# Kernel tuning notes

Measured on AMD Instinct MI355X. Metric: run time of the kernel, lower is better.

Reference implementation:

```python
import jax, jax.numpy as jnp
import numpy as np

NHEAD = 4
NLAYERS = 4
C = 128
EPS = 1e-5


def ln(x, g, b):
    m = x.mean(-1, keepdims=True)
    v = jnp.var(x, axis=-1, keepdims=True)
    return (x - m) / jnp.sqrt(v + EPS) * g + b


def mha_rel(q_in, k_in, in_w, in_b, out_w, out_b, pos_enc, pos_idx, self_attn):
    # q_in/k_in: [W, N, C]; pos_enc: [2W-1, C]; pos_idx: [W*W] int
    w, bsz, c = q_in.shape
    hd = c // NHEAD
    scale = hd ** -0.5
    if self_attn:
        qkv = q_in @ in_w.T + in_b
        q, k, v = jnp.split(qkv, 3, axis=-1)
    else:
        q = q_in @ in_w[:c].T + in_b[:c]
        kv = k_in @ in_w[c:].T + in_b[c:]
        k, v = jnp.split(kv, 2, axis=-1)
    pe = pos_enc[pos_idx].reshape(w, w, c)             # [W, W', C] gathered rel-pos
    qr_kr = pe @ in_w[:2 * c].T + in_b[:2 * c]
    q_r, k_r = jnp.split(qr_kr, 2, axis=-1)
    q = (q * scale).reshape(w, bsz, NHEAD, hd)
    q_r = (q_r * scale).reshape(w, w, NHEAD, hd)
    k = k.reshape(w, bsz, NHEAD, hd)
    v = v.reshape(w, bsz, NHEAD, hd)
    k_r = k_r.reshape(w, w, NHEAD, hd)
    # content-content + content-pos + pos-content (STTR MultiheadAttentionRelative)
    attn = (jnp.einsum('wnec,vnec->newv', q, k)
            + jnp.einsum('wnec,wvec->newv', q, k_r)
            + jnp.einsum('vnec,wvec->newv', k, q_r))   # [N, E, W, W']
    raw = attn.sum(1)
    a = jax.nn.softmax(attn, axis=-1)
    v_o = jnp.einsum('newv,vnec->wnec', a, v).reshape(w, bsz, c)
    v_o = v_o @ out_w.T + out_b
    return v_o, a.sum(1) / NHEAD, raw


def _forward(feat_left, feat_right, pos_enc,
             s_iw, s_ib, s_ow, s_ob, s_g, s_b,
             c_iw, c_ib, c_ow, c_ob, c_g1, c_b1, c_g2, c_b2):
    bs, c, hn0, w = feat_left.shape
    hn = hn0 * bs

    def to_seq(x):  # [bs,c,hn,w] -> [w, hn*bs, c]
        return jnp.transpose(jnp.transpose(x, (1, 3, 2, 0)).reshape(c, w, hn), (1, 2, 0))

    fl = to_seq(feat_left)
    fr = to_seq(feat_right)
    pos_idx = (jnp.arange(w - 1, -1, -1)[:, None] + jnp.arange(w)[None, :]).reshape(-1)
    pos_flip = pos_enc[::-1]
    feat = jnp.concatenate([fl, fr], axis=1)           # [w, 2hn, c]
    for i in range(NLAYERS):
        # self attention over concatenated left/right
        f2 = ln(feat, s_g[i], s_b[i])
        f2, _, _ = mha_rel(f2, f2, s_iw[i], s_ib[i], s_ow[i], s_ob[i], pos_enc, pos_idx, True)
        feat = feat + f2
        # cross attention
        fl, fr = feat[:, :hn], feat[:, hn:]
        fl2 = ln(fl, c_g1[i], c_b1[i])
        fr2 = ln(fr, c_g1[i], c_b1[i])
        fr2u, _, _ = mha_rel(fr2, fl2, c_iw[i], c_ib[i], c_ow[i], c_ob[i], pos_flip, pos_idx, False)
        fr = fr + fr2u
        fr2n = ln(fr, c_g2[i], c_b2[i])
        fl2u, _, _ = mha_rel(fl2, fr2n, c_iw[i], c_ib[i], c_ow[i], c_ob[i], pos_enc, pos_idx, False)
        fl = fl + fl2u
        feat = jnp.concatenate([fl, fr], axis=1)
    return feat


def setup_inputs() -> dict:
    key = jax.random.key(0)
    ks = jax.random.split(key, 20)
    bs, hn, w = 2, 64, 192
    p = 0.02
    return {
        "feat_left": jax.random.normal(ks[0], (bs, C, hn, w), jnp.float32),
        "feat_right": jax.random.normal(ks[1], (bs, C, hn, w), jnp.float32),
        "pos_enc": jax.random.normal(ks[2], (2 * w - 1, C), jnp.float32),
        "s_iw": jax.random.normal(ks[3], (NLAYERS, 3 * C, C), jnp.float32) * p,
        "s_ib": jax.random.normal(ks[4], (NLAYERS, 3 * C), jnp.float32) * p,
        "s_ow": jax.random.normal(ks[5], (NLAYERS, C, C), jnp.float32) * p,
        "s_ob": jax.random.normal(ks[6], (NLAYERS, C), jnp.float32) * p,
        "s_g": jnp.ones((NLAYERS, C), jnp.float32),
        "s_b": jnp.zeros((NLAYERS, C), jnp.float32),
        "c_iw": jax.random.normal(ks[7], (NLAYERS, 3 * C, C), jnp.float32) * p,
        "c_ib": jax.random.normal(ks[8], (NLAYERS, 3 * C), jnp.float32) * p,
        "c_ow": jax.random.normal(ks[9], (NLAYERS, C, C), jnp.float32) * p,
        "c_ob": jax.random.normal(ks[10], (NLAYERS, C), jnp.float32) * p,
        "c_g1": jnp.ones((NLAYERS, C), jnp.float32),
        "c_b1": jnp.zeros((NLAYERS, C), jnp.float32),
        "c_g2": jnp.ones((NLAYERS, C), jnp.float32),
        "c_b2": jnp.zeros((NLAYERS, C), jnp.float32),
    }


def reference(feat_left, feat_right, pos_enc,
              s_iw, s_ib, s_ow, s_ob, s_g, s_b,
              c_iw, c_ib, c_ow, c_ob, c_g1, c_b1, c_g2, c_b2):
    return _forward(feat_left, feat_right, pos_enc,
                    s_iw, s_ib, s_ow, s_ob, s_g, s_b,
                    c_iw, c_ib, c_ow, c_ob, c_g1, c_b1, c_g2, c_b2)
```

## Files before the change

### kernel.cpp

```cpp
#include <hip/hip_runtime.h>
#include <hip/hip_bf16.h>
#include <math.h>

#define WW 192
#define NTOT 256
#define HNN 128
#define CC 128
#define NH 4
#define NLAY 4
#define EPSF 1e-5f
#define SCALE 0.17677669529663687f

typedef __attribute__((ext_vector_type(8))) short short8_t;
typedef __attribute__((ext_vector_type(4))) float f32x4;

#define MFMA(a, b, c) __builtin_amdgcn_mfma_f32_16x16x32_bf16(a, b, c, 0, 0, 0)

__device__ __forceinline__ ushort f2b(float f) {
  union { float f; uint u; } x; x.f = f;
  uint r = x.u + 0x7fffu + ((x.u >> 16) & 1u);
  return (ushort)(r >> 16);
}

__global__ __launch_bounds__(256) void k_build_feat(const float* __restrict__ L,
                                                    const float* __restrict__ R,
                                                    float* __restrict__ feat) {
  __shared__ float tile[32][33];
  int wt = blockIdx.x, h0 = blockIdx.y, z = blockIdx.z;
  int ct = z & 3, b = (z >> 2) & 1, side = z >> 3;
  const float* src = side ? R : L;
  int tx = threadIdx.x & 31, ty = threadIdx.x >> 5;
  const float* sp = src + ((size_t)(b * 128 + ct * 32) * 64 + h0) * 192 + wt * 32;
  #pragma unroll
  for (int yy = 0; yy < 4; ++yy) {
    int c = ty * 4 + yy;
    tile[c][tx] = sp[(size_t)c * 64 * 192 + tx];
  }
  __syncthreads();
  int n = 2 * h0 + b + side * 128;
  #pragma unroll
  for (int yy = 0; yy < 4; ++yy) {
    int w = ty * 4 + yy;
    feat[((size_t)(wt * 32 + w) * 256 + n) * 128 + ct * 32 + tx] = tile[tx][w];
  }
}

__global__ __launch_bounds__(256) void k_gemm_mfma(
    const void* __restrict__ Xv, int lnmode, int xN, int x0,
    const float* __restrict__ lng, const float* __restrict__ lnb,
    const float* __restrict__ Wt, const float* __restrict__ bias,
    void* __restrict__ Yv, int yN, int y0, int ystride, int yf32res,
    int T, int nsub, float* __restrict__ Ymir) {
  extern __shared__ char smem[];
  ushort* As = (ushort*)smem;
  ushort* Bs = As + 128 * 128;
  float* biasS = (float*)(Bs + 128 * 128);

  int bm = blockIdx.x, bn = blockIdx.y;
  int tid = threadIdx.x;

  {
    int row = tid >> 1;
    int ce0 = (tid & 1) * 64;
    int t = bm * 128 + row;
    bool ok = (t < T);
    int w = 0, h = 0;
    if (ok) { w = t / nsub; h = t - w * nsub; }
    if (lnmode) {
      const float* src = (const float*)Xv + (size_t)(w * xN + x0 + h) * CC + ce0;
      float vals[64];
      float s = 0.f, s2 = 0.f;
      #pragma unroll
      for (int i = 0; i < 16; ++i) {
        float4 v = ok ? *(const float4*)(src + i * 4) : make_float4(0.f, 0.f, 0.f, 0.f);
        vals[i * 4 + 0] = v.x; vals[i * 4 + 1] = v.y;
        vals[i * 4 + 2] = v.z; vals[i * 4 + 3] = v.w;
        s += v.x + v.y + v.z + v.w;
        s2 += v.x * v.x + v.y * v.y + v.z * v.z + v.w * v.w;
      }
      s += __shfl_xor(s, 1);
      s2 += __shfl_xor(s2, 1);
      float m = s * (1.0f / 128.0f);
      float inv = rsqrtf(s2 * (1.0f / 128.0f) - m * m + EPSF);
      #pragma unroll
      for (int i = 0; i < 8; ++i) {
        float4 g0 = *(const float4*)(lng + ce0 + i * 8);
        float4 g1 = *(const float4*)(lng + ce0 + i * 8 + 4);
        float4 b0 = *(const float4*)(lnb + ce0 + i * 8);
        float4 b1 = *(const float4*)(lnb + ce0 + i * 8 + 4);
        short8_t pv;
        pv[0] = (short)f2b((vals[i * 8 + 0] - m) * inv * g0.x + b0.x);
        pv[1] = (short)f2b((vals[i * 8 + 1] - m) * inv * g0.y + b0.y);
        pv[2] = (short)f2b((vals[i * 8 + 2] - m) * inv * g0.z + b0.z);
        pv[3] = (short)f2b((vals[i * 8 + 3] - m) * inv * g0.w + b0.w);
        pv[4] = (short)f2b((vals[i * 8 + 4] - m) * inv * g1.x + b1.x);
        pv[5] = (short)f2b((vals[i * 8 + 5] - m) * inv * g1.y + b1.y);
        pv[6] = (short)f2b((vals[i * 8 + 6] - m) * inv * g1.z + b1.z);
        pv[7] = (short)f2b((vals[i * 8 + 7] - m) * inv * g1.w + b1.w);
        int cb = (ce0 + i * 8) * 2;
        *(short8_t*)((char*)As + row * 256 + (cb ^ ((row & 7) << 4))) = pv;
      }
    } else {
      const ushort* src = (const ushort*)Xv + (size_t)(w * xN + x0 + h) * CC + ce0;
      #pragma unroll
      for (int i = 0; i < 8; ++i) {
        short8_t v = {};
        if (ok) v = *(const short8_t*)(src + i * 8);
        int cb = (ce0 + i * 8) * 2;
        *(short8_t*)((char*)As + row * 256 + (cb ^ ((row & 7) << 4))) = v;
      }
    }
    const float* wsrc = Wt + (size_t)(bn * 128 + row) * CC + ce0;
    #pragma unroll
    for (int i = 0; i < 8; ++i) {
      float4 v0 = *(const float4*)(wsrc + i * 8);
      float4 v1 = *(const float4*)(wsrc + i * 8 + 4);
      short8_t pv;
      pv[0] = (short)f2b(v0.x); pv[1] = (short)f2b(v0.y);
      pv[2] = (short)f2b(v0.z); pv[3] = (short)f2b(v0.w);
      pv[4] = (short)f2b(v1.x); pv[5] = (short)f2b(v1.y);
      pv[6] = (short)f2b(v1.z); pv[7] = (short)f2b(v1.w);
      int cb = (ce0 + i * 8) * 2;
      *(short8_t*)((char*)Bs + row * 256 + (cb ^ ((row & 7) << 4))) = pv;
    }
    if (tid < 128) biasS[tid] = bias[bn * 128 + tid];
  }
  __syncthreads();

  int lane = tid & 63, wid = tid >> 6;
  int wm = (wid >> 1) * 64, wn = (wid & 1) * 64;
  int r = lane & 15, g = lane >> 4;

  f32x4 acc[4][4] = {};
  #pragma unroll
  for (int kc = 0; kc < 4; ++kc) {
    short8_t af[4], bf[4];
    #pragma unroll
    for (int mt = 0; mt < 4; ++mt) {
      int row = wm + mt * 16 + r;
      af[mt] = *(const short8_t*)((const char*)As + row * 256 + ((kc * 64 + g * 16) ^ ((row & 7) << 4)));
    }
    #pragma unroll
    for (int nt = 0; nt < 4; ++nt) {
      int row = wn + nt * 16 + r;
      bf[nt] = *(const short8_t*)((const char*)Bs + row * 256 + ((kc * 64 + g * 16) ^ ((row & 7) << 4)));
    }
    __builtin_amdgcn_s_setprio(1);
    #pragma unroll
    for (int mt = 0; mt < 4; ++mt)
      #pragma unroll
      for (int nt = 0; nt < 4; ++nt)
        acc[mt][nt] = MFMA(af[mt], bf[nt], acc[mt][nt]);
    __builtin_amdgcn_s_setprio(0);
  }

  #pragma unroll
  for (int mt = 0; mt < 4; ++mt) {
    #pragma unroll
    for (int reg = 0; reg < 4; ++reg) {
      int t = bm * 128 + wm + mt * 16 + g * 4 + reg;
      if (t < T) {
        int w = t / nsub, h = t - w * nsub;
        size_t ybase = (size_t)(w * yN + y0 + h) * ystride + bn * 128;
        #pragma unroll
        for (int nt = 0; nt < 4; ++nt) {
          int nn = wn + nt * 16 + r;
          float v = acc[mt][nt][reg] + biasS[nn];
          if (yf32res) {
            float nv = ((float*)Yv)[ybase + nn] + v;
            ((float*)Yv)[ybase + nn] = nv;
            if (Ymir) Ymir[ybase + nn] = nv;
          } else {
            ((ushort*)Yv)[ybase + nn] = f2b(v);
          }
        }
      }
    }
  }
}

__global__ __launch_bounds__(256) void k_rr(
    const float* __restrict__ pos_enc,
    const float* __restrict__ s_iw, const float* __restrict__ s_ib,
    const float* __restrict__ c_iw, const float* __restrict__ c_ib,
    ushort* __restrict__ out_all) {
  extern __shared__ char smem[];
  ushort* As = (ushort*)smem;
  ushort* Bs = As + 128 * 128;
  float* biasS = (float*)(Bs + 128 * 128);

  int bm = blockIdx.x, bn = blockIdx.y, z = blockIdx.z;
  int layer = z >> 1;
  const float* Wt = ((z & 1) ? c_iw : s_iw) + (size_t)layer * 384 * CC;
  const float* bias = ((z & 1) ? c_ib : s_ib) + layer * 384;
  ushort* out = out_all + (size_t)z * 383 * 256;
  int tid = threadIdx.x;

  {
    int row = tid >> 1;
    int ce0 = (tid & 1) * 64;
    int t = bm * 128 + row;
    bool ok = (t < 383);
    const float* src = pos_enc + (size_t)t * CC + ce0;
    #pragma unroll
    for (int i = 0; i < 8; ++i) {
      float4 v0 = ok ? *(const float4*)(src + i * 8) : make_float4(0.f, 0.f, 0.f, 0.f);
      float4 v1 = ok ? *(const float4*)(src + i * 8 + 4) : make_float4(0.f, 0.f, 0.f, 0.f);
      short8_t pv;
      pv[0] = (short)f2b(v0.x); pv[1] = (short)f2b(v0.y);
      pv[2] = (short)f2b(v0.z); pv[3] = (short)f2b(v0.w);
      pv[4] = (short)f2b(v1.x); pv[5] = (short)f2b(v1.y);
      pv[6] = (short)f2b(v1.z); pv[7] = (short)f2b(v1.w);
      int cb = (ce0 + i * 8) * 2;
      *(short8_t*)((char*)As + row * 256 + (cb ^ ((row & 7) << 4))) = pv;
    }
    const float* wsrc = Wt + (size_t)(bn * 128 + row) * CC + ce0;
    #pragma unroll
    for (int i = 0; i < 8; ++i) {
      float4 v0 = *(const float4*)(wsrc + i * 8);
      float4 v1 = *(const float4*)(wsrc + i * 8 + 4);
      short8_t pv;
      pv[0] = (short)f2b(v0.x); pv[1] = (short)f2b(v0.y);
      pv[2] = (short)f2b(v0.z); pv[3] = (short)f2b(v0.w);
      pv[4] = (short)f2b(v1.x); pv[5] = (short)f2b(v1.y);
      pv[6] = (short)f2b(v1.z); pv[7] = (short)f2b(v1.w);
      int cb = (ce0 + i * 8) * 2;
      *(short8_t*)((char*)Bs + row * 256 + (cb ^ ((row & 7) << 4))) = pv;
    }
    if (tid < 128) biasS[tid] = bias[bn * 128 + tid];
  }
  __syncthreads();

  int lane = tid & 63, wid = tid >> 6;
  int wm = (wid >> 1) * 64, wn = (wid & 1) * 64;
  int r = lane & 15, g = lane >> 4;

  f32x4 acc[4][4] = {};
  #pragma unroll
  for (int kc = 0; kc < 4; ++kc) {
    short8_t af[4], bf[4];
    #pragma unroll
    for (int mt = 0; mt < 4; ++mt) {
      int row = wm + mt * 16 + r;
      af[mt] = *(const short8_t*)((const char*)As + row * 256 + ((kc * 64 + g * 16) ^ ((row & 7) << 4)));
    }
    #pragma unroll
    for (int nt = 0; nt < 4; ++nt) {
      int row = wn + nt * 16 + r;
      bf[nt] = *(const short8_t*)((const char*)Bs + row * 256 + ((kc * 64 + g * 16) ^ ((row & 7) << 4)));
    }
    #pragma unroll
    for (int mt = 0; mt < 4; ++mt)
      #pragma unroll
      for (int nt = 0; nt < 4; ++nt)
        acc[mt][nt] = MFMA(af[mt], bf[nt], acc[mt][nt]);
  }

  #pragma unroll
  for (int mt = 0; mt < 4; ++mt) {
    #pragma unroll
    for (int reg = 0; reg < 4; ++reg) {
      int t = bm * 128 + wm + mt * 16 + g * 4 + reg;
      if (t < 383) {
        #pragma unroll
        for (int nt = 0; nt < 4; ++nt) {
          int nn = wn + nt * 16 + r;
          out[(size_t)t * 256 + bn * 128 + nn] = f2b(acc[mt][nt][reg] + biasS[nn]);
        }
      }
    }
  }
}

#define KS_ST 36
#define VT_ST 196
#define B2_ST 37
#define PL_ST 20

template <int SGN>
__global__ __launch_bounds__(256, 4) void k_attn_mfma(
    const ushort* __restrict__ qbuf, int qstride, int qoff, int qN, int qn0,
    const ushort* __restrict__ kvbuf, int kvstride, int koff, int voff, int kN, int kn0,
    const ushort* __restrict__ rrb,
    ushort* __restrict__ obuf, int oN,
    int nblk) {
  __shared__ ushort Ks[192 * KS_ST];
  __shared__ ushort Vt[32 * VT_ST];
  __shared__ float Sb[4 * 16 * B2_ST];
  __shared__ uint PLb[4 * 16 * PL_ST];

  int bid = blockIdx.x;
  int n = bid % nblk;
  int rest = bid / nblk;
  int h = rest & 3;
  int ts = rest >> 2;
  int tid = threadIdx.x;
  int lane = tid & 63, wid = tid >> 6;
  int r = lane & 15, g = lane >> 4;
  int g4 = g * 4;

  for (int i = tid; i < 768; i += 256) {
    int row = i >> 2, c8 = (i & 3) * 8;
    *(short8_t*)&Ks[row * KS_ST + c8] =
        *(const short8_t*)(kvbuf + (size_t)(row * kN + kn0 + n) * kvstride + koff + h * 32 + c8);
  }
  {
    uint* Vtu = (uint*)Vt;
    for (int i = tid; i < 384; i += 256) {
      int dg = i / 96;
      int p = i - dg * 96;
      const ushort* vb = kvbuf + (size_t)((2 * p) * kN + kn0 + n) * kvstride + voff + h * 32 + dg * 8;
      short8_t a = *(const short8_t*)vb;
      short8_t b = *(const short8_t*)(vb + (size_t)kN * kvstride);
      #pragma unroll
      for (int j = 0; j < 8; ++j)
        Vtu[(dg * 8 + j) * 98 + p] = ((uint)(ushort)a[j]) | (((uint)(ushort)b[j]) << 16);
    }
  }
  int w0 = (ts * 4 + wid) * 16;
  short8_t qf = *(const short8_t*)(qbuf + (size_t)((w0 + r) * qN + qn0 + n) * qstride + qoff + h * 32 + g * 8);
  __syncthreads();

  float* flat = Sb + wid * 16 * B2_ST;
  uint* PL = PLb + wid * 16 * PL_ST;
  const ushort* KRg = rrb + 128 + h * 32 + g * 8;
  const ushort* QRg = rrb + h * 32 + g * 8;
  const f32x4 zf = {0.f, 0.f, 0.f, 0.f};

  int ca = (SGN < 0) ? (r + 1) : (31 - r);
  int cbn = (SGN < 0) ? (17 + r) : (15 - r);
  int rdcol = 16 - r + g4;

  f32x4 esum = zf, o0 = zf, o1 = zf;

  #pragma unroll
  for (int vp = 0; vp < 6; ++vp) {
    #pragma unroll
    for (int half = 0; half < 2; ++half) {
      int s = 2 * vp + half;
      int v0 = s * 16;
      short8_t kf = *(const short8_t*)&Ks[(v0 + r) * KS_ST + g * 8];
      int base2 = 176 + SGN * (w0 - v0);
      const ushort* krp = KRg + (size_t)(base2 + r) * 256;
      const ushort* qrp = QRg + (size_t)(base2 + r) * 256;
      short8_t krf0 = *(const short8_t*)krp;
      short8_t krf1 = *(const short8_t*)(krp + 16 * 256);
      short8_t qrf0 = *(const short8_t*)qrp;
      short8_t qrf1 = *(const short8_t*)(qrp + 16 * 256);
      __builtin_amdgcn_s_setprio(1);
      f32x4 t1  = MFMA(kf, qf, zf);
      f32x4 t3a = MFMA(kf, qrf0, zf);
      f32x4 t3b = MFMA(kf, qrf1, zf);
      f32x4 t2a = MFMA(qf, krf0, zf);
      f32x4 t2b = MFMA(qf, krf1, zf);
      __builtin_amdgcn_s_setprio(0);
      #pragma unroll
      for (int reg = 0; reg < 4; ++reg) {
        flat[(g4 + reg) * B2_ST + ca] = t2a[reg];
        flat[(g4 + reg) * B2_ST + cbn] = t2b[reg];
      }
      f32x4 p2v = *(const f32x4*)&flat[r * B2_ST + rdcol];
      f32x4 ev;
      #pragma unroll
      for (int reg = 0; reg < 4; ++reg) {
        int js = 15 + SGN * (r - g4 - reg);
        int idx = (lane & 48) | (js & 15);
        float v3a = __shfl(t3a[reg], idx);
        float v3b = __shfl(t3b[reg], idx);
        float p3 = (js < 16) ? v3a : v3b;
        float e = __expf((t1[reg] + p2v[reg] + p3) * SCALE);
        ev[reg] = e;
        esum[reg] += e;
      }
      uint pa = (uint)f2b(ev[0]) | ((uint)f2b(ev[1]) << 16);
      uint pbu = (uint)f2b(ev[2]) | ((uint)f2b(ev[3]) << 16);
      *(uint2*)&PL[r * PL_ST + 8 * half + 2 * g] = make_uint2(pa, pbu);
    }
    union { uint u[4]; short8_t s8; } pb;
    uint4 pr = *(const uint4*)&PL[r * PL_ST + 4 * g];
    pb.u[0] = pr.x; pb.u[1] = pr.y; pb.u[2] = pr.z; pb.u[3] = pr.w;
    short8_t vt0 = *(const short8_t*)&Vt[r * VT_ST + vp * 32 + g * 8];
    short8_t vt1 = *(const short8_t*)&Vt[(16 + r) * VT_ST + vp * 32 + g * 8];
    __builtin_amdgcn_s_setprio(1);
    o0 = MFMA(vt0, pb.s8, o0);
    o1 = MFMA(vt1, pb.s8, o1);
    __builtin_amdgcn_s_setprio(0);
  }

  float ssum = (esum[0] + esum[1]) + (esum[2] + esum[3]);
  ssum += __shfl_xor(ssum, 16);
  ssum += __shfl_xor(ssum, 32);

  float inv = 1.0f / ssum;
  ushort4 u0, u1;
  u0.x = f2b(o0[0] * inv); u0.y = f2b(o0[1] * inv);
  u0.z = f2b(o0[2] * inv); u0.w = f2b(o0[3] * inv);
  u1.x = f2b(o1[0] * inv); u1.y = f2b(o1[1] * inv);
  u1.z = f2b(o1[2] * inv); u1.w = f2b(o1[3] * inv);
  size_t rowb = (size_t)((w0 + r) * oN + n) * CC + h * 32;
  *(ushort4*)(obuf + rowb + g4) = u0;
  *(ushort4*)(obuf + rowb + 16 + g4) = u1;
}

extern "C" void kernel_launch(void* const* d_in, const int* in_sizes, int n_in,
                              void* d_out, int out_size, void* d_ws, size_t ws_size,
                              hipStream_t stream) {
  const float* feat_left  = (const float*)d_in[0];
  const float* feat_right = (const float*)d_in[1];
  const float* pos_enc    = (const float*)d_in[2];
  const float* s_iw = (const float*)d_in[3];
  const float* s_ib = (const float*)d_in[4];
  const float* s_ow = (const float*)d_in[5];
  const float* s_ob = (const float*)d_in[6];
  const float* s_g  = (const float*)d_in[7];
  const float* s_b  = (const float*)d_in[8];
  const float* c_iw = (const float*)d_in[9];
  const float* c_ib = (const float*)d_in[10];
  const float* c_ow = (const float*)d_in[11];
  const float* c_ob = (const float*)d_in[12];
  const float* c_g1 = (const float*)d_in[13];
  const float* c_b1 = (const float*)d_in[14];
  const float* c_g2 = (const float*)d_in[15];
  const float* c_b2 = (const float*)d_in[16];

  char* W = (char*)d_ws;
  const int FEAT_N = WW * NTOT * CC;
  float*  feat    = (float*)W;
  ushort* qkv     = (ushort*)(W + 25165824);
  ushort* obuf    = (ushort*)(W + 62914560);
  ushort* kv2     = (ushort*)(W + 75497472);
  ushort* rrb_all = (ushort*)(W + 88080384);

  const int GEMM_LDS = 128 * 128 * 2 * 2 + 128 * 4;
  hipFuncSetAttribute(reinterpret_cast<const void*>(&k_gemm_mfma),
                      hipFuncAttributeMaxDynamicSharedMemorySize, GEMM_LDS);
  hipFuncSetAttribute(reinterpret_cast<const void*>(&k_rr),
                      hipFuncAttributeMaxDynamicSharedMemorySize, GEMM_LDS);

  k_build_feat<<<dim3(6, 64, 16), 256, 0, stream>>>(feat_left, feat_right, feat);
  k_rr<<<dim3(3, 2, 8), 256, GEMM_LDS, stream>>>(pos_enc, s_iw, s_ib, c_iw, c_ib, rrb_all);

  const int T_FULL = WW * NTOT;
  const int T_HALF = WW * HNN;

  for (int i = 0; i < NLAY; ++i) {
    const float* siw = s_iw + (size_t)i * 384 * CC;
    const float* sib = s_ib + i * 384;
    const float* sow = s_ow + (size_t)i * CC * CC;
    const float* sob = s_ob + i * CC;
    const float* ciw = c_iw + (size_t)i * 384 * CC;
    const float* cib = c_ib + i * 384;
    const float* cow = c_ow + (size_t)i * CC * CC;
    const float* cob = c_ob + i * CC;
    const ushort* rr_self  = rrb_all + (size_t)(2 * i) * 383 * 256;
    const ushort* rr_cross = rrb_all + (size_t)(2 * i + 1) * 383 * 256;
    float* mir = (i == NLAY - 1) ? (float*)d_out : nullptr;

    k_gemm_mfma<<<dim3(T_FULL / 128, 3), 256, GEMM_LDS, stream>>>(
        feat, 1, NTOT, 0, s_g + i * CC, s_b + i * CC, siw, sib,
        qkv, NTOT, 0, 384, 0, T_FULL, NTOT, nullptr);
    k_attn_mfma<-1><<<NTOT * NH * 3, 256, 0, stream>>>(
        qkv, 384, 0, NTOT, 0, qkv, 384, 128, 256, NTOT, 0,
        rr_self, obuf, NTOT, NTOT);
    k_gemm_mfma<<<dim3(T_FULL / 128, 1), 256, GEMM_LDS, stream>>>(
        obuf, 0, NTOT, 0, nullptr, nullptr, sow, sob,
        feat, NTOT, 0, CC, 1, T_FULL, NTOT, nullptr);

    k_gemm_mfma<<<dim3(T_FULL / 128, 3), 256, GEMM_LDS, stream>>>(
        feat, 1, NTOT, 0, c_g1 + i * CC, c_b1 + i * CC, ciw, cib,
        qkv, NTOT, 0, 384, 0, T_FULL, NTOT, nullptr);

    k_attn_mfma<+1><<<HNN * NH * 3, 256, 0, stream>>>(
        qkv, 384, 0, NTOT, 128, qkv, 384, 128, 256, NTOT, 0,
        rr_cross, obuf, HNN, HNN);
    k_gemm_mfma<<<dim3(T_HALF / 128, 1), 256, GEMM_LDS, stream>>>(
        obuf, 0, HNN, 0, nullptr, nullptr, cow, cob,
        feat, NTOT, 128, CC, 1, T_HALF, HNN, mir);

    k_gemm_mfma<<<dim3(T_HALF / 128, 2), 256, GEMM_LDS, stream>>>(
        feat, 1, NTOT, 128, c_g2 + i * CC, c_b2 + i * CC, ciw + 128 * CC, cib + 128,
        kv2, HNN, 0, 256, 0, T_HALF, HNN, nullptr);
    k_attn_mfma<-1><<<HNN * NH * 3, 256, 0, stream>>>(
        qkv, 384, 0, NTOT, 0, kv2, 256, 0, 128, HNN, 0,
        rr_cross, obuf, HNN, HNN);
    k_gemm_mfma<<<dim3(T_HALF / 128, 1), 256, GEMM_LDS, stream>>>(
        obuf, 0, HNN, 0, nullptr, nullptr, cow, cob,
        feat, NTOT, 0, CC, 1, T_HALF, HNN, mir);
  }
}
```

Baseline: 1.497 ms.

## Pre-convert weights to bf16 and split LayerNorm out of GEMM

Adds a one-time kernel that converts all projection weights to bf16, so GEMM blocks load bf16 weights directly instead of converting fp32 per block. LayerNorm moves out of the GEMM prologue into a separate k_ln kernel that writes a bf16 normalized buffer, which the GEMM then reads. This drops redundant per-block weight conversion and LN recompute across the column blocks, but adds extra launches and a bf16 activation round-trip through memory.

Measured after the change: 1.382 ms. 1.08x faster.

```diff
diff --git a/kernel.cpp b/kernel.cpp
--- a/kernel.cpp
+++ b/kernel.cpp
@@ -45,10 +45,53 @@
   }
 }
 
-__global__ __launch_bounds__(256) void k_gemm_mfma(
-    const void* __restrict__ Xv, int lnmode, int xN, int x0,
-    const float* __restrict__ lng, const float* __restrict__ lnb,
-    const float* __restrict__ Wt, const float* __restrict__ bias,
+__global__ __launch_bounds__(256) void k_wconv(
+    const float* __restrict__ s_iw, const float* __restrict__ s_ow,
+    const float* __restrict__ c_iw, const float* __restrict__ c_ow,
+    ushort* __restrict__ out) {
+  int i4 = (blockIdx.x * 256 + threadIdx.x) * 4;
+  const float* src;
+  int off;
+  if (i4 < 196608) { src = s_iw; off = i4; }
+  else if (i4 < 262144) { src = s_ow; off = i4 - 196608; }
+  else if (i4 < 458752) { src = c_iw; off = i4 - 262144; }
+  else { src = c_ow; off = i4 - 458752; }
+  float4 v = *(const float4*)(src + off);
+  ushort4 o;
+  o.x = f2b(v.x); o.y = f2b(v.y); o.z = f2b(v.z); o.w = f2b(v.w);
+  *(ushort4*)(out + i4) = o;
+}
+
+__global__ __launch_bounds__(256) void k_ln(const float* __restrict__ src,
+                                            ushort* __restrict__ dst,
+                                            const float* __restrict__ g,
+                                            const float* __restrict__ b,
+                                            int n0, int nsub) {
+  int t = blockIdx.x * 4 + (threadIdx.x >> 6);
+  int lane = threadIdx.x & 63;
+  int w = t / nsub, h = t - w * nsub;
+  size_t row = (size_t)(w * NTOT + n0 + h) * CC;
+  int c0 = lane * 2;
+  float2 x = *(const float2*)(src + row + c0);
+  float s = x.x + x.y;
+  float s2 = x.x * x.x + x.y * x.y;
+  #pragma unroll
+  for (int o = 1; o < 64; o <<= 1) {
+    s += __shfl_xor(s, o);
+    s2 += __shfl_xor(s2, o);
+  }
+  float m = s * (1.0f / 128.0f);
+  float var = s2 * (1.0f / 128.0f) - m * m;
+  float inv = rsqrtf(var + EPSF);
+  float oa = (x.x - m) * inv * g[c0] + b[c0];
+  float ob = (x.y - m) * inv * g[c0 + 1] + b[c0 + 1];
+  uint pack = (uint)f2b(oa) | ((uint)f2b(ob) << 16);
+  *(uint*)(dst + row + c0) = pack;
+}
+
+__global__ __launch_bounds__(256) void k_gemm_bf16(
+    const ushort* __restrict__ X, int xN, int x0,
+    const ushort* __restrict__ Wb, const float* __restrict__ bias,
     void* __restrict__ Yv, int yN, int y0, int ystride, int yf32res,
     int T, int nsub, float* __restrict__ Ymir) {
   extern __shared__ char smem[];
@@ -66,62 +109,20 @@
     bool ok = (t < T);
     int w = 0, h = 0;
     if (ok) { w = t / nsub; h = t - w * nsub; }
-    if (lnmode) {
-      const float* src = (const float*)Xv + (size_t)(w * xN + x0 + h) * CC + ce0;
-      float vals[64];
-      float s = 0.f, s2 = 0.f;
-      #pragma unroll
-      for (int i = 0; i < 16; ++i) {
-        float4 v = ok ? *(const float4*)(src + i * 4) : make_float4(0.f, 0.f, 0.f, 0.f);
-        vals[i * 4 + 0] = v.x; vals[i * 4 + 1] = v.y;
-        vals[i * 4 + 2] = v.z; vals[i * 4 + 3] = v.w;
-        s += v.x + v.y + v.z + v.w;
-        s2 += v.x * v.x + v.y * v.y + v.z * v.z + v.w * v.w;
-      }
-      s += __shfl_xor(s, 1);
-      s2 += __shfl_xor(s2, 1);
-      float m = s * (1.0f / 128.0f);
-      float inv = rsqrtf(s2 * (1.0f / 128.0f) - m * m + EPSF);
-      #pragma unroll
-      for (int i = 0; i < 8; ++i) {
-        float4 g0 = *(const float4*)(lng + ce0 + i * 8);
-        float4 g1 = *(const float4*)(lng + ce0 + i * 8 + 4);
-        float4 b0 = *(const float4*)(lnb + ce0 + i * 8);
-        float4 b1 = *(const float4*)(lnb + ce0 + i * 8 + 4);
-        short8_t pv;
-        pv[0] = (short)f2b((vals[i * 8 + 0] - m) * inv * g0.x + b0.x);
-        pv[1] = (short)f2b((vals[i * 8 + 1] - m) * inv * g0.y + b0.y);
-        pv[2] = (short)f2b((vals[i * 8 + 2] - m) * inv * g0.z + b0.z);
-        pv[3] = (short)f2b((vals[i * 8 + 3] - m) * inv * g0.w + b0.w);
-        pv[4] = (short)f2b((vals[i * 8 + 4] - m) * inv * g1.x + b1.x);
-        pv[5] = (short)f2b((vals[i * 8 + 5] - m) * inv * g1.y + b1.y);
-        pv[6] = (short)f2b((vals[i * 8 + 6] - m) * inv * g1.z + b1.z);
-        pv[7] = (short)f2b((vals[i * 8 + 7] - m) * inv * g1.w + b1.w);
-        int cb = (ce0 + i * 8) * 2;
-        *(short8_t*)((char*)As + row * 256 + (cb ^ ((row & 7) << 4))) = pv;
-      }
-    } else {
-      const ushort* src = (const ushort*)Xv + (size_t)(w * xN + x0 + h) * CC + ce0;
-      #pragma unroll
-      for (int i = 0; i < 8; ++i) {
-        short8_t v = {};
-        if (ok) v = *(const short8_t*)(src + i * 8);
-        int cb = (ce0 + i * 8) * 2;
-        *(short8_t*)((char*)As + row * 256 + (cb ^ ((row & 7) << 4))) = v;
-      }
-    }
-    const float* wsrc = Wt + (size_t)(bn * 128 + row) * CC + ce0;
+    const ushort* src = X + (size_t)(w * xN + x0 + h) * CC + ce0;
     #pragma unroll
     for (int i = 0; i < 8; ++i) {
-      float4 v0 = *(const float4*)(wsrc + i * 8);
-      float4 v1 = *(const float4*)(wsrc + i * 8 + 4);
-      short8_t pv;
-      pv[0] = (short)f2b(v0.x); pv[1] = (short)f2b(v0.y);
-      pv[2] = (short)f2b(v0.z); pv[3] = (short)f2b(v0.w);
-      pv[4] = (short)f2b(v1.x); pv[5] = (short)f2b(v1.y);
-      pv[6] = (short)f2b(v1.z); pv[7] = (short)f2b(v1.w);
+      short8_t v = {};
+      if (ok) v = *(const short8_t*)(src + i * 8);
       int cb = (ce0 + i * 8) * 2;
-      *(short8_t*)((char*)Bs + row * 256 + (cb ^ ((row & 7) << 4))) = pv;
+      *(short8_t*)((char*)As + row * 256 + (cb ^ ((row & 7) << 4))) = v;
+    }
+    const ushort* wsrc = Wb + (size_t)(bn * 128 + row) * CC + ce0;
+    #pragma unroll
+    for (int i = 0; i < 8; ++i) {
+      short8_t v = *(const short8_t*)(wsrc + i * 8);
+      int cb = (ce0 + i * 8) * 2;
+      *(short8_t*)((char*)Bs + row * 256 + (cb ^ ((row & 7) << 4))) = v;
     }
     if (tid < 128) biasS[tid] = bias[bn * 128 + tid];
   }
@@ -426,65 +427,72 @@
   char* W = (char*)d_ws;
   const int FEAT_N = WW * NTOT * CC;
   float*  feat    = (float*)W;
-  ushort* qkv     = (ushort*)(W + 25165824);
-  ushort* obuf    = (ushort*)(W + 62914560);
+  ushort* f2obuf  = (ushort*)(W + 25165824);
+  ushort* qkv     = (ushort*)(W + 37748736);
   ushort* kv2     = (ushort*)(W + 75497472);
   ushort* rrb_all = (ushort*)(W + 88080384);
+  ushort* wbf     = (ushort*)(W + 89649152);
+
+  ushort* f2   = f2obuf;
+  ushort* obuf = f2obuf;
 
   const int GEMM_LDS = 128 * 128 * 2 * 2 + 128 * 4;
-  hipFuncSetAttribute(reinterpret_cast<const void*>(&k_gemm_mfma),
+  hipFuncSetAttribute(reinterpret_cast<const void*>(&k_gemm_bf16),
                       hipFuncAttributeMaxDynamicSharedMemorySize, GEMM_LDS);
   hipFuncSetAttribute(reinterpret_cast<const void*>(&k_rr),
                       hipFuncAttributeMaxDynamicSharedMemorySize, GEMM_LDS);
 
   k_build_feat<<<dim3(6, 64, 16), 256, 0, stream>>>(feat_left, feat_right, feat);
   k_rr<<<dim3(3, 2, 8), 256, GEMM_LDS, stream>>>(pos_enc, s_iw, s_ib, c_iw, c_ib, rrb_all);
+  k_wconv<<<512, 256, 0, stream>>>(s_iw, s_ow, c_iw, c_ow, wbf);
+
+  const ushort* siw_bf_base = wbf;
+  const ushort* sow_bf_base = wbf + 196608;
+  const ushort* ciw_bf_base = wbf + 262144;
+  const ushort* cow_bf_base = wbf + 458752;
 
   const int T_FULL = WW * NTOT;
   const int T_HALF = WW * HNN;
 
   for (int i = 0; i < NLAY; ++i) {
-    const float* siw = s_iw + (size_t)i * 384 * CC;
     const float* sib = s_ib + i * 384;
-    const float* sow = s_ow + (size_t)i * CC * CC;
     const float* sob = s_ob + i * CC;
-    const float* ciw = c_iw + (size_t)i * 384 * CC;
     const float* cib = c_ib + i * 384;
-    const float* cow = c_ow + (size_t)i * CC * CC;
     const float* cob = c_ob + i * CC;
+    const ushort* siw_bf = siw_bf_base + (size_t)i * 384 * CC;
+    const ushort* sow_bf = sow_bf_base + (size_t)i * CC * CC;
+    const ushort* ciw_bf = ciw_bf_base + (size_t)i * 384 * CC;
+    const ushort* cow_bf = cow_bf_base + (size_t)i * CC * CC;
     const ushort* rr_self  = rrb_all + (size_t)(2 * i) * 383 * 256;
     const ushort* rr_cross = rrb_all + (size_t)(2 * i + 1) * 383 * 256;
     float* mir = (i == NLAY - 1) ? (float*)d_out : nullptr;
 
-    k_gemm_mfma<<<dim3(T_FULL / 128, 3), 256, GEMM_LDS, stream>>>(
-        feat, 1, NTOT, 0, s_g + i * CC, s_b + i * CC, siw, sib,
-        qkv, NTOT, 0, 384, 0, T_FULL, NTOT, nullptr);
+    k_ln<<<T_FULL / 4, 256, 0, stream>>>(feat, f2, s_g + i * CC, s_b + i * CC, 0, NTOT);
+    k_gemm_bf16<<<dim3(T_FULL / 128, 3), 256, GEMM_LDS, stream>>>(
+        f2, NTOT, 0, siw_bf, sib, qkv, NTOT, 0, 384, 0, T_FULL, NTOT, nullptr);
     k_attn_mfma<-1><<<NTOT * NH * 3, 256, 0, stream>>>(
         qkv, 384, 0, NTOT, 0, qkv, 384, 128, 256, NTOT, 0,
         rr_self, obuf, NTOT, NTOT);
-    k_gemm_mfma<<<dim3(T_FULL / 128, 1), 256, GEMM_LDS, stream>>>(
-        obuf, 0, NTOT, 0, nullptr, nullptr, sow, sob,
-        feat, NTOT, 0, CC, 1, T_FULL, NTOT, nullptr);
-
-    k_gemm_mfma<<<dim3(T_FULL / 128, 3), 256, GEMM_LDS, stream>>>(
-        feat, 1, NTOT, 0, c_g1 + i * CC, c_b1 + i * CC, ciw, cib,
-        qkv, NTOT, 0, 384, 0, T_FULL, NTOT, nullptr);
+    k_gemm_bf16<<<dim3(T_FULL / 128, 1), 256, GEMM_LDS, stream>>>(
+        obuf, NTOT, 0, sow_bf, sob, feat, NTOT, 0, CC, 1, T_FULL, NTOT, nullptr);
+
+    k_ln<<<T_FULL / 4, 256, 0, stream>>>(feat, f2, c_g1 + i * CC, c_b1 + i * CC, 0, NTOT);
+    k_gemm_bf16<<<dim3(T_FULL / 128, 3), 256, GEMM_LDS, stream>>>(
+        f2, NTOT, 0, ciw_bf, cib, qkv, NTOT, 0, 384, 0, T_FULL, NTOT, nullptr);
 
     k_attn_mfma<+1><<<HNN * NH * 3, 256, 0, stream>>>(
         qkv, 384, 0, NTOT, 128, qkv, 384, 128, 256, NTOT, 0,
         rr_cross, obuf, HNN, HNN);
-    k_gemm_mfma<<<dim3(T_HALF / 128, 1), 256, GEMM_LDS, stream>>>(
-        obuf, 0, HNN, 0, nullptr, nullptr, cow, cob,
-        feat, NTOT, 128, CC, 1, T_HALF, HNN, mir);
-
-    k_gemm_mfma<<<dim3(T_HALF / 128, 2), 256, GEMM_LDS, stream>>>(
-        feat, 1, NTOT, 128, c_g2 + i * CC, c_b2 + i * CC, ciw + 128 * CC, cib + 128,
-        kv2, HNN, 0, 256, 0, T_HALF, HNN, nullptr);
+    k_gemm_bf16<<<dim3(T_HALF / 128, 1), 256, GEMM_LDS, stream>>>(
+        obuf, HNN, 0, cow_bf, cob, feat, NTOT, 128, CC, 1, T_HALF, HNN, mir);
+
+    k_ln<<<T_HALF / 4, 256, 0, stream>>>(feat, f2, c_g2 + i * CC, c_b2 + i * CC, 128, HNN);
+    k_gemm_bf16<<<dim3(T_HALF / 128, 2), 256, GEMM_LDS, stream>>>(
+        f2, NTOT, 128, ciw_bf + 128 * CC, cib + 128, kv2, HNN, 0, 256, 0, T_HALF, HNN, nullptr);
     k_attn_mfma<-1><<<HNN * NH * 3, 256, 0, stream>>>(
         qkv, 384, 0, NTOT, 0, kv2, 256, 0, 128, HNN, 0,
         rr_cross, obuf, HNN, HNN);
-    k_gemm_mfma<<<dim3(T_HALF / 128, 1), 256, GEMM_LDS, stream>>>(
-        obuf, 0, HNN, 0, nullptr, nullptr, cow, cob,
-        feat, NTOT, 0, CC, 1, T_HALF, HNN, mir);
-  }
-}
+    k_gemm_bf16<<<dim3(T_HALF / 128, 1), 256, GEMM_LDS, stream>>>(
+        obuf, HNN, 0, cow_bf, cob, feat, NTOT, 0, CC, 1, T_HALF, HNN, mir);
+  }
+}
```
